# Performance work log

Measured on AMD Instinct MI355X. Metric: run time of the kernel, lower is better.

The kernel has to match this reference:

```python
import jax, jax.numpy as jnp
import numpy as np

NUM_HEADS = 12
TEMPORAL_RES = 8


def _ln(x, g, b, eps=1e-5):
    mu = jnp.mean(x, axis=-1, keepdims=True)
    var = jnp.mean((x - mu) ** 2, axis=-1, keepdims=True)
    return (x - mu) * jax.lax.rsqrt(var + eps) * g + b


def setup_inputs() -> dict:
    key = jax.random.key(0)
    ks = jax.random.split(key, 8)
    s = 0.02
    d = 768
    inp = {
        'box_tensors': jax.random.uniform(ks[0], (16, 16, 10, 4), dtype=jnp.float32),
        'box_categories': jax.random.normal(ks[1], (16, 10, d), dtype=jnp.float32) * s,
        'w1': jax.random.normal(ks[2], (4, d // 2), dtype=jnp.float32) * s,
        'w2': jax.random.normal(ks[3], (d // 2, d), dtype=jnp.float32) * s,
        'ln1_g': jnp.ones((d,), jnp.float32),
        'ln1_b': jnp.zeros((d,), jnp.float32),
        'wqkv': jax.random.normal(ks[4], (d, 3 * d), dtype=jnp.float32) * s,
        'wo': jax.random.normal(ks[5], (d, d), dtype=jnp.float32) * s,
        'bo': jnp.zeros((d,), jnp.float32),
        'ln2_g': jnp.ones((d,), jnp.float32),
        'ln2_b': jnp.zeros((d,), jnp.float32),
        'wfc1': jax.random.normal(ks[6], (d, 4 * d), dtype=jnp.float32) * s,
        'bfc1': jnp.zeros((4 * d,), jnp.float32),
        'wfc2': jax.random.normal(ks[7], (4 * d, d), dtype=jnp.float32) * s,
        'bfc2': jnp.zeros((d,), jnp.float32),
        'H': 14,
        'W': 14,
    }
    return inp


def _forward(box_tensors, box_categories, w1, w2, ln1_g, ln1_b, wqkv, wo, bo,
             ln2_g, ln2_b, wfc1, bfc1, wfc2, bfc2, H, W):
    B, T, O, _ = box_tensors.shape
    d = box_categories.shape[-1]
    # coord -> feature MLP (no biases), then pos-emb add
    h = jax.nn.relu(box_tensors @ w1)
    x = jax.nn.relu(h @ w2)                      # [B,T,O,d]
    x = x + box_categories[None]                 # broadcast over batch
    L = T * O
    x = x.reshape(B, L, d)
    # --- self-attention block (pre-LN ViT style) ---
    hn = _ln(x, ln1_g, ln1_b)
    qkv = (hn @ wqkv).reshape(B, L, 3, NUM_HEADS, d // NUM_HEADS)
    q, k, v = qkv[:, :, 0], qkv[:, :, 1], qkv[:, :, 2]   # [B,L,h,dh]
    scale = 1.0 / jnp.sqrt(jnp.asarray(d // NUM_HEADS, x.dtype))
    att = jnp.einsum('bqhd,bkhd->bhqk', q, k) * scale
    att = jax.nn.softmax(att, axis=-1)
    o = jnp.einsum('bhqk,bkhd->bqhd', att, v).reshape(B, L, d)
    x = x + (o @ wo + bo)
    hn = _ln(x, ln2_g, ln2_b)
    x = x + (jax.nn.gelu(hn @ wfc1 + bfc1, approximate=False) @ wfc2 + bfc2)
    feats = x.reshape(B, T, O, d)
    # --- box2spatial layout scatter: sum each object's feature into grid cells inside its box ---
    x1 = jnp.minimum(box_tensors[..., 0], box_tensors[..., 2])
    x2 = jnp.maximum(box_tensors[..., 0], box_tensors[..., 2])
    y1 = jnp.minimum(box_tensors[..., 1], box_tensors[..., 3])
    y2 = jnp.maximum(box_tensors[..., 1], box_tensors[..., 3])
    cy = (jnp.arange(H, dtype=x.dtype) + 0.5) / H    # [H]
    cx = (jnp.arange(W, dtype=x.dtype) + 0.5) / W    # [W]
    in_y = (cy[None, None, None, :] >= y1[..., None]) & (cy[None, None, None, :] <= y2[..., None])  # [B,T,O,H]
    in_x = (cx[None, None, None, :] >= x1[..., None]) & (cx[None, None, None, :] <= x2[..., None])  # [B,T,O,W]
    mask = (in_y[..., :, None] & in_x[..., None, :]).astype(x.dtype)  # [B,T,O,H,W]
    grid = jnp.einsum('btohw,btod->bthwd', mask, feats)               # [B,T,H,W,d]
    # temporal avg pooling to TEMPORAL_RES frames
    Tr = T // TEMPORAL_RES
    if Tr > 1:
        grid = grid.reshape(B, T // Tr, Tr, H, W, d).mean(axis=2)
    return grid.reshape(B, -1, d)                 # [B, T'*H*W, d]


def reference(box_tensors, box_categories, w1, w2, ln1_g, ln1_b, wqkv, wo, bo,
              ln2_g, ln2_b, wfc1, bfc1, wfc2, bfc2, H, W):
    return _forward(box_tensors, box_categories, w1, w2, ln1_g, ln1_b, wqkv, wo, bo,
                    ln2_g, ln2_b, wfc1, bfc1, wfc2, bfc2, H, W)
```

## Files before the change

### kernel.cpp

```cpp
#include <hip/hip_runtime.h>
#include <hip/hip_bf16.h>
#include <math.h>


#define BATCH 16
#define TT    16
#define OO    10
#define LL    160
#define BL    2560
#define DD    768
#define NH    12
#define DH    64
#define GH    14
#define GW    14
#define TGRP  8

typedef unsigned short ushort_t;
typedef __attribute__((ext_vector_type(8))) __bf16 bf16x8;
typedef __attribute__((ext_vector_type(4))) float f32x4;

__device__ __forceinline__ ushort_t f2bf(float f) {
    unsigned int u = __float_as_uint(f);
    u += 0x7fffu + ((u >> 16) & 1u);
    return (ushort_t)(u >> 16);
}

__global__ __launch_bounds__(256)
void transpose_w(const float* __restrict__ W, ushort_t* __restrict__ Wt, int K, int N)
{
    __shared__ float s[32][33];
    const int n0 = blockIdx.x * 32, k0 = blockIdx.y * 32;
    const int tx = threadIdx.x & 31, ty = threadIdx.x >> 5;
#pragma unroll
    for (int r = 0; r < 4; ++r)
        s[ty + r * 8][tx] = W[(size_t)(k0 + ty + r * 8) * N + n0 + tx];
    __syncthreads();
#pragma unroll
    for (int r = 0; r < 4; ++r)
        Wt[(size_t)(n0 + ty + r * 8) * K + k0 + tx] = f2bf(s[tx][ty + r * 8]);
}

__global__ __launch_bounds__(256)
void box_mlp(const float* __restrict__ box, const float* __restrict__ cat,
             const float* __restrict__ w1, const float* __restrict__ w2,
             float* __restrict__ x)
{
    __shared__ float hbuf[8][384];
    const int r0 = blockIdx.x * 8;
    const int tid = threadIdx.x;

#pragma unroll
    for (int k = 0; k < 12; ++k) {
        int idx = tid + k * 256;
        int i = idx / 384, j = idx - i * 384;
        const float* bx = box + (size_t)(r0 + i) * 4;
        float v = bx[0] * w1[j] + bx[1] * w1[384 + j] +
                  bx[2] * w1[768 + j] + bx[3] * w1[1152 + j];
        hbuf[i][j] = fmaxf(v, 0.f);
    }
    __syncthreads();

    float acc[8][3];
#pragma unroll
    for (int i = 0; i < 8; ++i) { acc[i][0] = 0.f; acc[i][1] = 0.f; acc[i][2] = 0.f; }

    for (int j = 0; j < 384; ++j) {
        const float wa = w2[(size_t)j * DD + tid];
        const float wb = w2[(size_t)j * DD + tid + 256];
        const float wc = w2[(size_t)j * DD + tid + 512];
#pragma unroll
        for (int i = 0; i < 8; ++i) {
            float hv = hbuf[i][j];
            acc[i][0] += hv * wa; acc[i][1] += hv * wb; acc[i][2] += hv * wc;
        }
    }

#pragma unroll
    for (int i = 0; i < 8; ++i) {
        int r = r0 + i;
        int to = r % LL;
        const float* cp = cat + (size_t)to * DD;
        float* xp = x + (size_t)r * DD;
        xp[tid]       = fmaxf(acc[i][0], 0.f) + cp[tid];
        xp[tid + 256] = fmaxf(acc[i][1], 0.f) + cp[tid + 256];
        xp[tid + 512] = fmaxf(acc[i][2], 0.f) + cp[tid + 512];
    }
}

__global__ __launch_bounds__(256)
void ln_kernel(const float* __restrict__ in, const float* __restrict__ g,
               const float* __restrict__ bvec, ushort_t* __restrict__ out)
{
    const int r = blockIdx.x;
    const int tid = threadIdx.x;
    const float* row = in + (size_t)r * DD;
    float v0 = row[tid], v1 = row[tid + 256], v2 = row[tid + 512];
    float s  = v0 + v1 + v2;
    float s2 = v0 * v0 + v1 * v1 + v2 * v2;
#pragma unroll
    for (int off = 32; off > 0; off >>= 1) {
        s  += __shfl_down(s, off);
        s2 += __shfl_down(s2, off);
    }
    __shared__ float red[8];
    int wave = tid >> 6, lane = tid & 63;
    if (lane == 0) { red[wave] = s; red[wave + 4] = s2; }
    __syncthreads();
    s  = red[0] + red[1] + red[2] + red[3];
    s2 = red[4] + red[5] + red[6] + red[7];
    float mu  = s * (1.f / DD);
    float var = s2 * (1.f / DD) - mu * mu;
    float inv = rsqrtf(var + 1e-5f);
    ushort_t* op = out + (size_t)r * DD;
    op[tid]       = f2bf((v0 - mu) * inv * g[tid]       + bvec[tid]);
    op[tid + 256] = f2bf((v1 - mu) * inv * g[tid + 256] + bvec[tid + 256]);
    op[tid + 512] = f2bf((v2 - mu) * inv * g[tid + 512] + bvec[tid + 512]);
}

template <int MODE>
__global__ __launch_bounds__(256)
void gemm_mfma(const ushort_t* __restrict__ A, int lda,
               const ushort_t* __restrict__ Bt, int ldb,
               const float* __restrict__ bias,
               float* __restrict__ Cf, ushort_t* __restrict__ Cb,
               int ldc, int K)
{
    __shared__ ushort_t As[128 * 32];
    __shared__ ushort_t Bs[128 * 32];
    const int tid  = threadIdx.x;
    const int wave = tid >> 6, lane = tid & 63;
    const int wr = wave >> 1, wc = wave & 1;
    const int row0 = blockIdx.y * 128, col0 = blockIdx.x * 128;

    f32x4 acc[4][4];
#pragma unroll
    for (int i = 0; i < 4; ++i)
#pragma unroll
        for (int j = 0; j < 4; ++j) {
            acc[i][j][0] = 0.f; acc[i][j][1] = 0.f;
            acc[i][j][2] = 0.f; acc[i][j][3] = 0.f;
        }

    const int srow = lane >> 2;
    const int scol = (lane & 3) * 8;
    const int q8 = (lane >> 4) * 8;
    const int mr = lane & 15;

    for (int kt = 0; kt < K; kt += 32) {
#pragma unroll
        for (int t = 0; t < 2; ++t) {
            const int inst = wave * 2 + t;
            const ushort_t* ga = A + (size_t)(row0 + inst * 16 + srow) * lda + kt + scol;
            __builtin_amdgcn_global_load_lds(
                (const __attribute__((address_space(1))) void*)ga,
                (__attribute__((address_space(3))) void*)&As[inst * 512], 16, 0, 0);
            const ushort_t* gb = Bt + (size_t)(col0 + inst * 16 + srow) * ldb + kt + scol;
            __builtin_amdgcn_global_load_lds(
                (const __attribute__((address_space(1))) void*)gb,
                (__attribute__((address_space(3))) void*)&Bs[inst * 512], 16, 0, 0);
        }
        __syncthreads();

        bf16x8 af[4], bfr[4];
#pragma unroll
        for (int i = 0; i < 4; ++i)
            af[i] = *reinterpret_cast<const bf16x8*>(&As[(wr * 64 + i * 16 + mr) * 32 + q8]);
#pragma unroll
        for (int j = 0; j < 4; ++j)
            bfr[j] = *reinterpret_cast<const bf16x8*>(&Bs[(wc * 64 + j * 16 + mr) * 32 + q8]);
#pragma unroll
        for (int i = 0; i < 4; ++i)
#pragma unroll
            for (int j = 0; j < 4; ++j)
                acc[i][j] = __builtin_amdgcn_mfma_f32_16x16x32_bf16(af[i], bfr[j], acc[i][j], 0, 0, 0);
        __syncthreads();
    }

    const int q4 = (lane >> 4) * 4;
#pragma unroll
    for (int i = 0; i < 4; ++i)
#pragma unroll
        for (int j = 0; j < 4; ++j) {
            const int gcol = col0 + wc * 64 + j * 16 + mr;
            const float bj = (MODE == 1 || MODE == 2) ? bias[gcol] : 0.f;
#pragma unroll
            for (int r = 0; r < 4; ++r) {
                const int grow = row0 + wr * 64 + i * 16 + q4 + r;
                const size_t idx = (size_t)grow * ldc + gcol;
                const float v = acc[i][j][r];
                if (MODE == 1) {
                    Cf[idx] += v + bj;
                } else if (MODE == 2) {
                    const float u = v + bj;
                    Cb[idx] = f2bf(0.5f * u * (1.f + erff(u * 0.70710678118654752f)));
                } else {
                    Cb[idx] = f2bf(v);
                }
            }
        }
}

#define KS_STRIDE 72
#define VT_STRIDE 168
__global__ __launch_bounds__(320)
void attention_mfma(const ushort_t* __restrict__ qkv, ushort_t* __restrict__ ao)
{
    __shared__ ushort_t Ks[160 * KS_STRIDE];
    __shared__ ushort_t Vt[64 * VT_STRIDE];
    __shared__ ushort_t Pb[5][32 * VT_STRIDE];

    const int b  = blockIdx.x / NH;
    const int hh = blockIdx.x % NH;
    const ushort_t* base = qkv + (size_t)b * LL * (3 * DD) + hh * DH;
    const int tid  = threadIdx.x;
    const int wave = tid >> 6, lane = tid & 63;
    const int l16 = lane & 15, quad = lane >> 4;

#pragma unroll
    for (int it = 0; it < 4; ++it) {
        int idx = tid + it * 320;
        int l = idx >> 3, c8 = (idx & 7) * 8;
        uint4 kv = *(const uint4*)(base + (size_t)l * (3 * DD) + DD + c8);
        *(uint4*)&Ks[l * KS_STRIDE + c8] = kv;
        uint4 vv = *(const uint4*)(base + (size_t)l * (3 * DD) + 2 * DD + c8);
        ushort_t e[8];
        *(uint4*)e = vv;
#pragma unroll
        for (int i = 0; i < 8; ++i)
            Vt[(c8 + i) * VT_STRIDE + l] = e[i];
    }

    const int q0 = wave * 32;
    bf16x8 qf[2][2];
#pragma unroll
    for (int t = 0; t < 2; ++t)
#pragma unroll
        for (int k = 0; k < 2; ++k)
            qf[t][k] = *reinterpret_cast<const bf16x8*>(
                base + (size_t)(q0 + t * 16 + l16) * (3 * DD) + k * 32 + quad * 8);

    __syncthreads();

    f32x4 S0[10], S1[10];
#pragma unroll
    for (int nt = 0; nt < 10; ++nt) {
        f32x4 z = {0.f, 0.f, 0.f, 0.f};
        const ushort_t* kb = &Ks[(nt * 16 + l16) * KS_STRIDE + quad * 8];
        bf16x8 kf0 = *reinterpret_cast<const bf16x8*>(kb);
        bf16x8 kf1 = *reinterpret_cast<const bf16x8*>(kb + 32);
        f32x4 a0 = __builtin_amdgcn_mfma_f32_16x16x32_bf16(qf[0][0], kf0, z, 0, 0, 0);
        S0[nt]   = __builtin_amdgcn_mfma_f32_16x16x32_bf16(qf[0][1], kf1, a0, 0, 0, 0);
        f32x4 a1 = __builtin_amdgcn_mfma_f32_16x16x32_bf16(qf[1][0], kf0, z, 0, 0, 0);
        S1[nt]   = __builtin_amdgcn_mfma_f32_16x16x32_bf16(qf[1][1], kf1, a1, 0, 0, 0);
    }

#pragma unroll
    for (int t = 0; t < 2; ++t) {
        f32x4* S = t ? S1 : S0;
        float mrow[4] = {-1e30f, -1e30f, -1e30f, -1e30f};
#pragma unroll
        for (int nt = 0; nt < 10; ++nt)
#pragma unroll
            for (int r = 0; r < 4; ++r) {
                S[nt][r] *= 0.125f;
                mrow[r] = fmaxf(mrow[r], S[nt][r]);
            }
#pragma unroll
        for (int r = 0; r < 4; ++r) {
            mrow[r] = fmaxf(mrow[r], __shfl_xor(mrow[r], 1));
            mrow[r] = fmaxf(mrow[r], __shfl_xor(mrow[r], 2));
            mrow[r] = fmaxf(mrow[r], __shfl_xor(mrow[r], 4));
            mrow[r] = fmaxf(mrow[r], __shfl_xor(mrow[r], 8));
        }
        float lsum[4] = {0.f, 0.f, 0.f, 0.f};
#pragma unroll
        for (int nt = 0; nt < 10; ++nt)
#pragma unroll
            for (int r = 0; r < 4; ++r) {
                float e = __expf(S[nt][r] - mrow[r]);
                S[nt][r] = e;
                lsum[r] += e;
            }
#pragma unroll
        for (int r = 0; r < 4; ++r) {
            lsum[r] += __shfl_xor(lsum[r], 1);
            lsum[r] += __shfl_xor(lsum[r], 2);
            lsum[r] += __shfl_xor(lsum[r], 4);
            lsum[r] += __shfl_xor(lsum[r], 8);
            lsum[r] = 1.f / lsum[r];
        }
#pragma unroll
        for (int nt = 0; nt < 10; ++nt)
#pragma unroll
            for (int r = 0; r < 4; ++r)
                Pb[wave][(t * 16 + quad * 4 + r) * VT_STRIDE + nt * 16 + l16] =
                    f2bf(S[nt][r] * lsum[r]);
    }
    asm volatile("s_waitcnt lgkmcnt(0)" ::: "memory");

#pragma unroll
    for (int dt = 0; dt < 4; ++dt) {
        f32x4 o0 = {0.f, 0.f, 0.f, 0.f}, o1 = {0.f, 0.f, 0.f, 0.f};
#pragma unroll
        for (int ks = 0; ks < 5; ++ks) {
            bf16x8 vf = *reinterpret_cast<const bf16x8*>(
                &Vt[(dt * 16 + l16) * VT_STRIDE + ks * 32 + quad * 8]);
            bf16x8 p0 = *reinterpret_cast<const bf16x8*>(
                &Pb[wave][(l16) * VT_STRIDE + ks * 32 + quad * 8]);
            bf16x8 p1 = *reinterpret_cast<const bf16x8*>(
                &Pb[wave][(16 + l16) * VT_STRIDE + ks * 32 + quad * 8]);
            o0 = __builtin_amdgcn_mfma_f32_16x16x32_bf16(vf, p0, o0, 0, 0, 0);
            o1 = __builtin_amdgcn_mfma_f32_16x16x32_bf16(vf, p1, o1, 0, 0, 0);
        }
#pragma unroll
        for (int t = 0; t < 2; ++t) {
            f32x4 o = t ? o1 : o0;
            ushort_t pk[4];
#pragma unroll
            for (int r = 0; r < 4; ++r) pk[r] = f2bf(o[r]);
            ushort_t* dst = ao + (size_t)(b * LL + q0 + t * 16 + l16) * DD +
                            hh * DH + dt * 16 + quad * 4;
            *(uint2*)dst = *(const uint2*)pk;
        }
    }
}

__global__ __launch_bounds__(256)
void mask_grid(const float* __restrict__ box, const float* __restrict__ feats,
               float* __restrict__ out)
{
    const int hw = blockIdx.x;
    const int g  = blockIdx.y;
    const int b  = blockIdx.z;
    const int hh = hw / GW, w = hw % GW;
    const float cy = (hh + 0.5f) / (float)GH;
    const float cx = (w  + 0.5f) / (float)GW;
    const int tid = threadIdx.x;

    __shared__ float flg[20];
    if (tid < 20) {
        int t = g * 2 + tid / OO, o = tid % OO;
        const float* bx = box + (size_t)((b * TT + t) * OO + o) * 4;
        float x1 = fminf(bx[0], bx[2]), x2 = fmaxf(bx[0], bx[2]);
        float y1 = fminf(bx[1], bx[3]), y2 = fmaxf(bx[1], bx[3]);
        flg[tid] = (cy >= y1 && cy <= y2 && cx >= x1 && cx <= x2) ? 1.f : 0.f;
    }
    __syncthreads();

    float a0 = 0.f, a1 = 0.f, a2 = 0.f;
#pragma unroll
    for (int p = 0; p < 20; ++p) {
        if (flg[p] != 0.f) {
            int r = (b * TT + g * 2 + p / OO) * OO + (p % OO);
            const float* f = feats + (size_t)r * DD;
            a0 += f[tid]; a1 += f[tid + 256]; a2 += f[tid + 512];
        }
    }
    float* op = out + ((size_t)b * (TGRP * GH * GW) + g * (GH * GW) + hw) * DD;
    op[tid]       = a0 * 0.5f;
    op[tid + 256] = a1 * 0.5f;
    op[tid + 512] = a2 * 0.5f;
}

extern "C" void kernel_launch(void* const* d_in, const int* in_sizes, int n_in,
                              void* d_out, int out_size, void* d_ws, size_t ws_size,
                              hipStream_t stream)
{
    const float* box  = (const float*)d_in[0];
    const float* cat  = (const float*)d_in[1];
    const float* w1   = (const float*)d_in[2];
    const float* w2   = (const float*)d_in[3];
    const float* ln1g = (const float*)d_in[4];
    const float* ln1b = (const float*)d_in[5];
    const float* wqkv = (const float*)d_in[6];
    const float* wo   = (const float*)d_in[7];
    const float* bo   = (const float*)d_in[8];
    const float* ln2g = (const float*)d_in[9];
    const float* ln2b = (const float*)d_in[10];
    const float* wfc1 = (const float*)d_in[11];
    const float* bfc1 = (const float*)d_in[12];
    const float* wfc2 = (const float*)d_in[13];
    const float* bfc2 = (const float*)d_in[14];
    float* out = (float*)d_out;

    char* wsb = (char*)d_ws;
    float*    x     = (float*)   (wsb + 0);
    ushort_t* qkvb  = (ushort_t*)(wsb + 7864320);
    ushort_t* fc1b  = qkvb;
    ushort_t* hnb   = (ushort_t*)(wsb + 23592960);
    ushort_t* aob   = (ushort_t*)(wsb + 27525120);
    ushort_t* wqkvT = (ushort_t*)(wsb + 31457280);
    ushort_t* woT   = (ushort_t*)(wsb + 34996224);
    ushort_t* wfc1T = (ushort_t*)(wsb + 36175872);
    ushort_t* wfc2T = (ushort_t*)(wsb + 40894464);

    transpose_w<<<dim3(2304 / 32, 768 / 32), 256, 0, stream>>>(wqkv, wqkvT, 768, 2304);
    transpose_w<<<dim3(768 / 32, 768 / 32), 256, 0, stream>>>(wo, woT, 768, 768);
    transpose_w<<<dim3(3072 / 32, 768 / 32), 256, 0, stream>>>(wfc1, wfc1T, 768, 3072);
    transpose_w<<<dim3(768 / 32, 3072 / 32), 256, 0, stream>>>(wfc2, wfc2T, 3072, 768);

    box_mlp<<<BL / 8, 256, 0, stream>>>(box, cat, w1, w2, x);
    ln_kernel<<<BL, 256, 0, stream>>>(x, ln1g, ln1b, hnb);
    gemm_mfma<3><<<dim3(18, 20), 256, 0, stream>>>(hnb, DD, wqkvT, DD, nullptr,
                                                   nullptr, qkvb, 3 * DD, DD);
    attention_mfma<<<BATCH * NH, 320, 0, stream>>>(qkvb, aob);
    gemm_mfma<1><<<dim3(6, 20), 256, 0, stream>>>(aob, DD, woT, DD, bo,
                                                  x, nullptr, DD, DD);
    ln_kernel<<<BL, 256, 0, stream>>>(x, ln2g, ln2b, hnb);
    gemm_mfma<2><<<dim3(24, 20), 256, 0, stream>>>(hnb, DD, wfc1T, DD, bfc1,
                                                   nullptr, fc1b, 4 * DD, DD);
    gemm_mfma<1><<<dim3(6, 20), 256, 0, stream>>>(fc1b, 4 * DD, wfc2T, 4 * DD, bfc2,
                                                  x, nullptr, DD, 4 * DD);
    mask_grid<<<dim3(GH * GW, TGRP, BATCH), 256, 0, stream>>>(box, x, out);
}
```

Measured before the change: 405.5 us.

## Replace LDS-tiled GEMM with register-direct single-wave GEMM, split-K, MFMA box MLP

Swaps the 128x128 LDS-staged 4-wave GEMM for a single-wave 64x64 kernel that loads bf16 fragments straight from global memory into registers with double buffering. The Wo and FC2 projections now use split-K with atomic accumulation to get more blocks. The box MLP second layer becomes a bf16 MFMA GEMM with a fused ReLU and category add. Attention writes its output in place into the Q slot of the qkv buffer, which removes a separate buffer. This gives more parallelism and no LDS barriers, at the cost of losing LDS data reuse across waves, making atomic-add results order-dependent, and running the box MLP in bf16 instead of fp32.

```diff
diff --git a/kernel.cpp b/kernel.cpp
--- a/kernel.cpp
+++ b/kernel.cpp
@@ -41,50 +41,15 @@
 }
 
 __global__ __launch_bounds__(256)
-void box_mlp(const float* __restrict__ box, const float* __restrict__ cat,
-             const float* __restrict__ w1, const float* __restrict__ w2,
-             float* __restrict__ x)
-{
-    __shared__ float hbuf[8][384];
-    const int r0 = blockIdx.x * 8;
-    const int tid = threadIdx.x;
-
-#pragma unroll
-    for (int k = 0; k < 12; ++k) {
-        int idx = tid + k * 256;
-        int i = idx / 384, j = idx - i * 384;
-        const float* bx = box + (size_t)(r0 + i) * 4;
-        float v = bx[0] * w1[j] + bx[1] * w1[384 + j] +
-                  bx[2] * w1[768 + j] + bx[3] * w1[1152 + j];
-        hbuf[i][j] = fmaxf(v, 0.f);
-    }
-    __syncthreads();
-
-    float acc[8][3];
-#pragma unroll
-    for (int i = 0; i < 8; ++i) { acc[i][0] = 0.f; acc[i][1] = 0.f; acc[i][2] = 0.f; }
-
-    for (int j = 0; j < 384; ++j) {
-        const float wa = w2[(size_t)j * DD + tid];
-        const float wb = w2[(size_t)j * DD + tid + 256];
-        const float wc = w2[(size_t)j * DD + tid + 512];
-#pragma unroll
-        for (int i = 0; i < 8; ++i) {
-            float hv = hbuf[i][j];
-            acc[i][0] += hv * wa; acc[i][1] += hv * wb; acc[i][2] += hv * wc;
-        }
-    }
-
-#pragma unroll
-    for (int i = 0; i < 8; ++i) {
-        int r = r0 + i;
-        int to = r % LL;
-        const float* cp = cat + (size_t)to * DD;
-        float* xp = x + (size_t)r * DD;
-        xp[tid]       = fmaxf(acc[i][0], 0.f) + cp[tid];
-        xp[tid + 256] = fmaxf(acc[i][1], 0.f) + cp[tid + 256];
-        xp[tid + 512] = fmaxf(acc[i][2], 0.f) + cp[tid + 512];
-    }
+void box_h(const float* __restrict__ box, const float* __restrict__ w1,
+           ushort_t* __restrict__ h)
+{
+    const int idx = blockIdx.x * 256 + threadIdx.x;
+    const int r = idx / 384, j = idx - r * 384;
+    const float* bx = box + (size_t)r * 4;
+    float v = bx[0] * w1[j] + bx[1] * w1[384 + j] +
+              bx[2] * w1[768 + j] + bx[3] * w1[1152 + j];
+    h[idx] = f2bf(fmaxf(v, 0.f));
 }
 
 __global__ __launch_bounds__(256)
@@ -117,20 +82,35 @@
     op[tid + 512] = f2bf((v2 - mu) * inv * g[tid + 512] + bvec[tid + 512]);
 }
 
-template <int MODE>
-__global__ __launch_bounds__(256)
-void gemm_mfma(const ushort_t* __restrict__ A, int lda,
-               const ushort_t* __restrict__ Bt, int ldb,
-               const float* __restrict__ bias,
-               float* __restrict__ Cf, ushort_t* __restrict__ Cb,
-               int ldc, int K)
-{
-    __shared__ ushort_t As[128 * 32];
-    __shared__ ushort_t Bs[128 * 32];
-    const int tid  = threadIdx.x;
-    const int wave = tid >> 6, lane = tid & 63;
-    const int wr = wave >> 1, wc = wave & 1;
-    const int row0 = blockIdx.y * 128, col0 = blockIdx.x * 128;
+#define LOADF(aa, bb, kk)                                                        \
+    _Pragma("unroll")                                                            \
+    for (int i = 0; i < 4; ++i) {                                                \
+        aa[i] = *reinterpret_cast<const bf16x8*>(ap + (size_t)(i * 16) * lda + (kk)); \
+        bb[i] = *reinterpret_cast<const bf16x8*>(bp + (size_t)(i * 16) * ldb + (kk)); \
+    }
+#define MFMA16(aa, bb)                                                           \
+    _Pragma("unroll")                                                            \
+    for (int i = 0; i < 4; ++i)                                                  \
+        _Pragma("unroll")                                                        \
+        for (int j = 0; j < 4; ++j)                                              \
+            acc[i][j] = __builtin_amdgcn_mfma_f32_16x16x32_bf16(aa[i], bb[j], acc[i][j], 0, 0, 0);
+
+template <int MODE, int SPLIT>
+__global__ __launch_bounds__(64)
+void gemm_rf(const ushort_t* __restrict__ A, int lda,
+             const ushort_t* __restrict__ Bt, int ldb,
+             const float* __restrict__ bias, const float* __restrict__ cat,
+             float* __restrict__ Cf, ushort_t* __restrict__ Cb,
+             int ldc, int K)
+{
+    const int lane = threadIdx.x;
+    const int l16 = lane & 15, quad = lane >> 4;
+    const int row0 = blockIdx.y * 64, col0 = blockIdx.x * 64;
+    const int Kper = K / SPLIT;
+    const int k0 = blockIdx.z * Kper;
+
+    const ushort_t* ap = A  + (size_t)(row0 + l16) * lda + k0 + quad * 8;
+    const ushort_t* bp = Bt + (size_t)(col0 + l16) * ldb + k0 + quad * 8;
 
     f32x4 acc[4][4];
 #pragma unroll
@@ -141,60 +121,43 @@
             acc[i][j][2] = 0.f; acc[i][j][3] = 0.f;
         }
 
-    const int srow = lane >> 2;
-    const int scol = (lane & 3) * 8;
-    const int q8 = (lane >> 4) * 8;
-    const int mr = lane & 15;
-
-    for (int kt = 0; kt < K; kt += 32) {
-#pragma unroll
-        for (int t = 0; t < 2; ++t) {
-            const int inst = wave * 2 + t;
-            const ushort_t* ga = A + (size_t)(row0 + inst * 16 + srow) * lda + kt + scol;
-            __builtin_amdgcn_global_load_lds(
-                (const __attribute__((address_space(1))) void*)ga,
-                (__attribute__((address_space(3))) void*)&As[inst * 512], 16, 0, 0);
-            const ushort_t* gb = Bt + (size_t)(col0 + inst * 16 + srow) * ldb + kt + scol;
-            __builtin_amdgcn_global_load_lds(
-                (const __attribute__((address_space(1))) void*)gb,
-                (__attribute__((address_space(3))) void*)&Bs[inst * 512], 16, 0, 0);
-        }
-        __syncthreads();
-
-        bf16x8 af[4], bfr[4];
-#pragma unroll
-        for (int i = 0; i < 4; ++i)
-            af[i] = *reinterpret_cast<const bf16x8*>(&As[(wr * 64 + i * 16 + mr) * 32 + q8]);
-#pragma unroll
-        for (int j = 0; j < 4; ++j)
-            bfr[j] = *reinterpret_cast<const bf16x8*>(&Bs[(wc * 64 + j * 16 + mr) * 32 + q8]);
-#pragma unroll
-        for (int i = 0; i < 4; ++i)
-#pragma unroll
-            for (int j = 0; j < 4; ++j)
-                acc[i][j] = __builtin_amdgcn_mfma_f32_16x16x32_bf16(af[i], bfr[j], acc[i][j], 0, 0, 0);
-        __syncthreads();
-    }
-
-    const int q4 = (lane >> 4) * 4;
+    bf16x8 a0[4], b0[4], a1[4], b1[4];
+    LOADF(a0, b0, 0)
+    int kt = 0;
+    for (; kt + 64 < Kper; kt += 64) {
+        LOADF(a1, b1, kt + 32)
+        MFMA16(a0, b0)
+        LOADF(a0, b0, kt + 64)
+        MFMA16(a1, b1)
+    }
+    LOADF(a1, b1, kt + 32)
+    MFMA16(a0, b0)
+    MFMA16(a1, b1)
+
+    const int q4 = quad * 4;
 #pragma unroll
     for (int i = 0; i < 4; ++i)
 #pragma unroll
         for (int j = 0; j < 4; ++j) {
-            const int gcol = col0 + wc * 64 + j * 16 + mr;
-            const float bj = (MODE == 1 || MODE == 2) ? bias[gcol] : 0.f;
+            const int gcol = col0 + j * 16 + l16;
+            const float bj = (MODE == 1 || MODE == 2)
+                               ? ((SPLIT == 1 || blockIdx.z == 0) ? bias[gcol] : 0.f)
+                               : 0.f;
 #pragma unroll
             for (int r = 0; r < 4; ++r) {
-                const int grow = row0 + wr * 64 + i * 16 + q4 + r;
+                const int grow = row0 + i * 16 + q4 + r;
                 const size_t idx = (size_t)grow * ldc + gcol;
                 const float v = acc[i][j][r];
                 if (MODE == 1) {
-                    Cf[idx] += v + bj;
+                    if (SPLIT > 1) atomicAdd(&Cf[idx], v + bj);
+                    else           Cf[idx] += v + bj;
                 } else if (MODE == 2) {
                     const float u = v + bj;
                     Cb[idx] = f2bf(0.5f * u * (1.f + erff(u * 0.70710678118654752f)));
+                } else if (MODE == 3) {
+                    Cb[idx] = f2bf(v);
                 } else {
-                    Cb[idx] = f2bf(v);
+                    Cf[idx] = fmaxf(v, 0.f) + cat[(size_t)(grow % LL) * DD + gcol];
                 }
             }
         }
@@ -203,7 +166,7 @@
 #define KS_STRIDE 72
 #define VT_STRIDE 168
 __global__ __launch_bounds__(320)
-void attention_mfma(const ushort_t* __restrict__ qkv, ushort_t* __restrict__ ao)
+void attention_mfma(ushort_t* __restrict__ qkv)
 {
     __shared__ ushort_t Ks[160 * KS_STRIDE];
     __shared__ ushort_t Vt[64 * VT_STRIDE];
@@ -211,7 +174,8 @@
 
     const int b  = blockIdx.x / NH;
     const int hh = blockIdx.x % NH;
-    const ushort_t* base = qkv + (size_t)b * LL * (3 * DD) + hh * DH;
+    ushort_t* basew = qkv + (size_t)b * LL * (3 * DD) + hh * DH;
+    const ushort_t* base = basew;
     const int tid  = threadIdx.x;
     const int wave = tid >> 6, lane = tid & 63;
     const int l16 = lane & 15, quad = lane >> 4;
@@ -318,8 +282,8 @@
             ushort_t pk[4];
 #pragma unroll
             for (int r = 0; r < 4; ++r) pk[r] = f2bf(o[r]);
-            ushort_t* dst = ao + (size_t)(b * LL + q0 + t * 16 + l16) * DD +
-                            hh * DH + dt * 16 + quad * 4;
+            ushort_t* dst = basew + (size_t)(q0 + t * 16 + l16) * (3 * DD) +
+                            dt * 16 + quad * 4;
             *(uint2*)dst = *(const uint2*)pk;
         }
     }
@@ -388,28 +352,32 @@
     ushort_t* qkvb  = (ushort_t*)(wsb + 7864320);
     ushort_t* fc1b  = qkvb;
     ushort_t* hnb   = (ushort_t*)(wsb + 23592960);
-    ushort_t* aob   = (ushort_t*)(wsb + 27525120);
-    ushort_t* wqkvT = (ushort_t*)(wsb + 31457280);
-    ushort_t* woT   = (ushort_t*)(wsb + 34996224);
-    ushort_t* wfc1T = (ushort_t*)(wsb + 36175872);
-    ushort_t* wfc2T = (ushort_t*)(wsb + 40894464);
+    ushort_t* wqkvT = (ushort_t*)(wsb + 27525120);
+    ushort_t* woT   = (ushort_t*)(wsb + 31064064);
+    ushort_t* wfc1T = (ushort_t*)(wsb + 32243712);
+    ushort_t* wfc2T = (ushort_t*)(wsb + 36962304);
+    ushort_t* w2T   = (ushort_t*)(wsb + 41680896);
+    ushort_t* h     = (ushort_t*)(wsb + 42270720);
 
     transpose_w<<<dim3(2304 / 32, 768 / 32), 256, 0, stream>>>(wqkv, wqkvT, 768, 2304);
     transpose_w<<<dim3(768 / 32, 768 / 32), 256, 0, stream>>>(wo, woT, 768, 768);
     transpose_w<<<dim3(3072 / 32, 768 / 32), 256, 0, stream>>>(wfc1, wfc1T, 768, 3072);
     transpose_w<<<dim3(768 / 32, 3072 / 32), 256, 0, stream>>>(wfc2, wfc2T, 3072, 768);
-
-    box_mlp<<<BL / 8, 256, 0, stream>>>(box, cat, w1, w2, x);
+    transpose_w<<<dim3(768 / 32, 384 / 32), 256, 0, stream>>>(w2, w2T, 384, 768);
+
+    box_h<<<BL * 384 / 256, 256, 0, stream>>>(box, w1, h);
+    gemm_rf<4, 1><<<dim3(12, 40, 1), 64, 0, stream>>>(h, 384, w2T, 384, nullptr, cat,
+                                                      x, nullptr, DD, 384);
     ln_kernel<<<BL, 256, 0, stream>>>(x, ln1g, ln1b, hnb);
-    gemm_mfma<3><<<dim3(18, 20), 256, 0, stream>>>(hnb, DD, wqkvT, DD, nullptr,
-                                                   nullptr, qkvb, 3 * DD, DD);
-    attention_mfma<<<BATCH * NH, 320, 0, stream>>>(qkvb, aob);
-    gemm_mfma<1><<<dim3(6, 20), 256, 0, stream>>>(aob, DD, woT, DD, bo,
-                                                  x, nullptr, DD, DD);
+    gemm_rf<3, 1><<<dim3(36, 40, 1), 64, 0, stream>>>(hnb, DD, wqkvT, DD, nullptr, nullptr,
+                                                      nullptr, qkvb, 3 * DD, DD);
+    attention_mfma<<<BATCH * NH, 320, 0, stream>>>(qkvb);
+    gemm_rf<1, 2><<<dim3(12, 40, 2), 64, 0, stream>>>(qkvb, 3 * DD, woT, DD, bo, nullptr,
+                                                      x, nullptr, DD, DD);
     ln_kernel<<<BL, 256, 0, stream>>>(x, ln2g, ln2b, hnb);
-    gemm_mfma<2><<<dim3(24, 20), 256, 0, stream>>>(hnb, DD, wfc1T, DD, bfc1,
-                                                   nullptr, fc1b, 4 * DD, DD);
-    gemm_mfma<1><<<dim3(6, 20), 256, 0, stream>>>(fc1b, 4 * DD, wfc2T, 4 * DD, bfc2,
-                                                  x, nullptr, DD, 4 * DD);
+    gemm_rf<2, 1><<<dim3(48, 40, 1), 64, 0, stream>>>(hnb, DD, wfc1T, DD, bfc1, nullptr,
+                                                      nullptr, fc1b, 4 * DD, DD);
+    gemm_rf<1, 4><<<dim3(12, 40, 4), 64, 0, stream>>>(fc1b, 4 * DD, wfc2T, 4 * DD, bfc2, nullptr,
+                                                      x, nullptr, DD, 4 * DD);
     mask_grid<<<dim3(GH * GW, TGRP, BATCH), 256, 0, stream>>>(box, x, out);
 }
```

Measured after the change: 370.2 us. -8.7%, faster.
